# Optimization experiments

Hardware: AMD Instinct MI355X
Metric: run time of the kernel (lower is better)

The kernel has to match this reference:

```python
import jax, jax.numpy as jnp
import numpy as np

FRAME, LATENT, HIDDEN, GATE_H, EXPERTS = 267, 32, 256, 64, 6
BATCH = 4096
IN0 = LATENT + FRAME            # 299: decoder layer-0 input (z, c)
IN1 = LATENT + HIDDEN           # 288: decoder layer-1/2 input (z, h)
OUT = FRAME                     # num_future_predictions * frame_size


def _lin(key, fan_in, fan_out):
    b = np.sqrt(1.0 / fan_in)
    return jax.random.uniform(key, (fan_in, fan_out), jnp.float32, -b, b)


def setup_inputs() -> dict:
    key = jax.random.key(0)
    ks = jax.random.split(key, 16)
    d = {
        "x": jax.random.normal(ks[0], (BATCH, FRAME), jnp.float32),
        "c": jax.random.normal(ks[1], (BATCH, FRAME), jnp.float32),
        "eps": jax.random.normal(ks[2], (BATCH, LATENT), jnp.float32),
        # encoder
        "enc_w1": _lin(ks[3], 2 * FRAME, HIDDEN), "enc_b1": jnp.zeros((HIDDEN,), jnp.float32),
        "enc_w2": _lin(ks[4], FRAME + HIDDEN, HIDDEN), "enc_b2": jnp.zeros((HIDDEN,), jnp.float32),
        "enc_wmu": _lin(ks[5], FRAME + HIDDEN, LATENT), "enc_bmu": jnp.zeros((LATENT,), jnp.float32),
        "enc_wlv": _lin(ks[6], FRAME + HIDDEN, LATENT), "enc_blv": jnp.zeros((LATENT,), jnp.float32),
        # gate MLP
        "g_w0": _lin(ks[7], IN0, GATE_H), "g_b0": jnp.zeros((GATE_H,), jnp.float32),
        "g_w1": _lin(ks[8], GATE_H, GATE_H), "g_b1": jnp.zeros((GATE_H,), jnp.float32),
        "g_w2": _lin(ks[9], GATE_H, EXPERTS), "g_b2": jnp.zeros((EXPERTS,), jnp.float32),
        # expert-mixed decoder layers (kaiming-uniform-ish init, bias 0.01)
        "w0": jax.random.uniform(ks[10], (EXPERTS, IN0, HIDDEN), jnp.float32, -np.sqrt(6.0 / IN0), np.sqrt(6.0 / IN0)),
        "b0": jnp.full((EXPERTS, HIDDEN), 0.01, jnp.float32),
        "w1": jax.random.uniform(ks[11], (EXPERTS, IN1, HIDDEN), jnp.float32, -np.sqrt(6.0 / IN1), np.sqrt(6.0 / IN1)),
        "b1": jnp.full((EXPERTS, HIDDEN), 0.01, jnp.float32),
        "w2": jax.random.uniform(ks[12], (EXPERTS, IN1, OUT), jnp.float32, -np.sqrt(6.0 / IN1), np.sqrt(6.0 / IN1)),
        "b2": jnp.full((EXPERTS, OUT), 0.01, jnp.float32),
    }
    return d


def reference(x, c, eps,
              enc_w1, enc_b1, enc_w2, enc_b2, enc_wmu, enc_bmu, enc_wlv, enc_blv,
              g_w0, g_b0, g_w1, g_b1, g_w2, g_b2,
              w0, b0, w1, b1, w2, b2):
    elu = jax.nn.elu
    # --- encoder ---
    h1 = elu(jnp.concatenate([x, c], axis=1) @ enc_w1 + enc_b1)
    h2 = elu(jnp.concatenate([x, h1], axis=1) @ enc_w2 + enc_b2)
    s = jnp.concatenate([x, h2], axis=1)
    mu = s @ enc_wmu + enc_bmu
    logvar = s @ enc_wlv + enc_blv
    z = mu + eps * jnp.exp(0.5 * logvar)
    # --- gate ---
    zc = jnp.concatenate([z, c], axis=1)
    g = elu(zc @ g_w0 + g_b0)
    g = elu(g @ g_w1 + g_b1)
    coeff = jax.nn.softmax(g @ g_w2 + g_b2, axis=1)  # [N, E]
    # --- soft-MoE decoder: blended-weight per-sample GEMMs ---
    layer = c
    for w, b, act in ((w0, b0, elu), (w1, b1, elu), (w2, b2, None)):
        inp = jnp.concatenate([z, layer], axis=1)  # [N, Din]
        # out[n,o] = sum_e coeff[n,e] * (inp[n,:] @ w[e,:,o]) + coeff[n,:] @ b[:,o]
        out = jnp.einsum('ne,ni,eio->no', coeff, inp, w) + coeff @ b
        layer = act(out) if act is not None else out
    return layer, mu, logvar
```

## Files before the change

### kernel.cpp

```cpp
#include <hip/hip_runtime.h>
#include <hip/hip_bf16.h>
#include <math.h>

#define N_BATCH 4096
#define FRAME   267
#define LATENT  32
#define HIDDEN  256
#define GATE_H  64
#define EXPERTS 6

typedef __hip_bfloat16 bf16;
typedef __bf16  bf16x8 __attribute__((ext_vector_type(8)));
typedef float   f32x4  __attribute__((ext_vector_type(4)));

__device__ __forceinline__ float eluf(float v) { return (v > 0.f) ? v : (expf(v) - 1.f); }

#define MFMA(a, b, p) __builtin_amdgcn_mfma_f32_16x16x32_bf16((a), (b), (p), 0, 0, 0)

struct WEnt { const float* src; bf16* dst; int K, M, Mtot, mOff, Ksteps, Mtiles, cum; };
struct WTab { WEnt e[10]; int total; };

__global__ __launch_bounds__(256) void prep_kernel(
    const float* __restrict__ bmu, const float* __restrict__ blv,
    float* __restrict__ biasCat, WTab tab)
{
    const int tid = threadIdx.x, bid = blockIdx.x;
    if (bid == 0 && tid < 64)
        biasCat[tid] = (tid < 32) ? bmu[tid] : blv[tid - 32];

    __shared__ float tbuf[32][33];
    int i = 0;
    while (i < 9 && bid >= tab.e[i + 1].cum) ++i;
    const WEnt en = tab.e[i];
    const int t = bid - en.cum;
    const int perE = en.Ksteps * en.Mtiles;
    const int e = t / perE;
    const int rr = t - e * perE;
    const int mt = rr / en.Ksteps;
    const int ks = rr - mt * en.Ksteps;
    const int tx = tid & 31, ty = tid >> 5;
    const float* src = en.src + (size_t)e * en.K * en.M;
    #pragma unroll
    for (int i0 = 0; i0 < 32; i0 += 8) {
        const int k = ks * 32 + i0 + ty, m = mt * 32 + tx;
        tbuf[i0 + ty][tx] = (k < en.K && m < en.M) ? src[(size_t)k * en.M + m] : 0.f;
    }
    __syncthreads();
    bf16* dst = en.dst + ((size_t)(e * en.Ksteps + ks) * en.Mtot + en.mOff + mt * 32) * 32;
    #pragma unroll
    for (int i0 = 0; i0 < 32; i0 += 8)
        dst[(size_t)(i0 + ty) * 32 + tx] = __float2bfloat16(tbuf[tx][i0 + ty]);
}

__global__ __launch_bounds__(1024, 4) void fused_kernel(
    const float* __restrict__ x, const float* __restrict__ c,
    const float* __restrict__ eps,
    const bf16* __restrict__ We1, const float* __restrict__ eb1,
    const bf16* __restrict__ We2, const float* __restrict__ eb2,
    const bf16* __restrict__ Wml, const float* __restrict__ biasCat,
    const bf16* __restrict__ Wg0, const float* __restrict__ gb0,
    const bf16* __restrict__ Wg1, const float* __restrict__ gb1,
    const bf16* __restrict__ Wg2, const float* __restrict__ gb2,
    const bf16* __restrict__ W0, const float* __restrict__ b0,
    const bf16* __restrict__ W1, const float* __restrict__ b1,
    const bf16* __restrict__ W2, const float* __restrict__ b2,
    float* __restrict__ out_layer, float* __restrict__ out_mu,
    float* __restrict__ out_lv)
{
    __shared__ bf16  bufA[16 * 552];
    __shared__ bf16  bufB[16 * 552];
    __shared__ float sML[16 * 64];
    __shared__ bf16  sG1[16 * 72];
    __shared__ bf16  sG2[16 * 72];
    __shared__ float sLg[16 * 16];
    __shared__ float sCo[EXPERTS * 16];

    const int tid  = threadIdx.x;
    const int w    = tid >> 6, lane = tid & 63, ml = lane & 15, quad = lane >> 4;
    const int row0 = blockIdx.x * 16;

    {
        const float* xr = x + (size_t)(row0 + w) * FRAME;
        const float* cr = c + (size_t)(row0 + w) * FRAME;
        #pragma unroll
        for (int j = 0; j < 9; ++j) {
            const int col = lane + j * 64;
            if (col < 544) {
                float v = 0.f;
                if (col < FRAME)          v = xr[col];
                else if (col < 2 * FRAME) v = cr[col - FRAME];
                bufA[w * 552 + col] = __float2bfloat16(v);
            }
        }
    }
    __syncthreads();

    {
        const int col = 16 * w + ml;
        f32x4 pa = (f32x4){0,0,0,0}, pb = (f32x4){0,0,0,0};
        const bf16* wp = We1 + (size_t)col * 32 + quad * 8;
        #pragma unroll
        for (int ks = 0; ks < 16; ks += 2) {
            const bf16x8 a0 = *(const bf16x8*)(bufA + ml * 552 + ks * 32 + quad * 8);
            const bf16x8 a1 = *(const bf16x8*)(bufA + ml * 552 + (ks + 1) * 32 + quad * 8);
            pa = MFMA(a0, *(const bf16x8*)(wp + (size_t)ks * 256 * 32), pa);
            pb = MFMA(a1, *(const bf16x8*)(wp + (size_t)(ks + 1) * 256 * 32), pb);
        }
        {
            const bf16x8 a16 = *(const bf16x8*)(bufA + ml * 552 + 16 * 32 + quad * 8);
            pa = MFMA(a16, *(const bf16x8*)(wp + (size_t)16 * 256 * 32), pa);
        }
        const float bv = eb1[col];
        #pragma unroll
        for (int rg = 0; rg < 4; ++rg)
            bufB[(quad * 4 + rg) * 552 + 267 + col] =
                __float2bfloat16(eluf(pa[rg] + pb[rg] + bv));
        #pragma unroll
        for (int j = 0; j < 5; ++j) {
            const int cc = lane + j * 64;
            if (cc < 267) bufB[w * 552 + cc] = bufA[w * 552 + cc];
        }
        if (lane < 21) bufB[w * 552 + 523 + lane] = __float2bfloat16(0.f);
    }
    __syncthreads();

    {
        const int col = 16 * w + ml;
        f32x4 pa = (f32x4){0,0,0,0}, pb = (f32x4){0,0,0,0};
        const bf16* wp = We2 + (size_t)col * 32 + quad * 8;
        #pragma unroll
        for (int ks = 0; ks < 16; ks += 2) {
            const bf16x8 a0 = *(const bf16x8*)(bufB + ml * 552 + ks * 32 + quad * 8);
            const bf16x8 a1 = *(const bf16x8*)(bufB + ml * 552 + (ks + 1) * 32 + quad * 8);
            pa = MFMA(a0, *(const bf16x8*)(wp + (size_t)ks * 256 * 32), pa);
            pb = MFMA(a1, *(const bf16x8*)(wp + (size_t)(ks + 1) * 256 * 32), pb);
        }
        {
            const bf16x8 a16 = *(const bf16x8*)(bufB + ml * 552 + 16 * 32 + quad * 8);
            pa = MFMA(a16, *(const bf16x8*)(wp + (size_t)16 * 256 * 32), pa);
        }
        __syncthreads();
        const float bv = eb2[col];
        #pragma unroll
        for (int rg = 0; rg < 4; ++rg)
            bufB[(quad * 4 + rg) * 552 + 267 + col] =
                __float2bfloat16(eluf(pa[rg] + pb[rg] + bv));
    }
    __syncthreads();

    if (w < 4) {
        const int col = 16 * w + ml;
        f32x4 pa = (f32x4){0,0,0,0}, pb = (f32x4){0,0,0,0};
        const bf16* wp = Wml + (size_t)col * 32 + quad * 8;
        #pragma unroll
        for (int ks = 0; ks < 16; ks += 2) {
            const bf16x8 a0 = *(const bf16x8*)(bufB + ml * 552 + ks * 32 + quad * 8);
            const bf16x8 a1 = *(const bf16x8*)(bufB + ml * 552 + (ks + 1) * 32 + quad * 8);
            pa = MFMA(a0, *(const bf16x8*)(wp + (size_t)ks * 64 * 32), pa);
            pb = MFMA(a1, *(const bf16x8*)(wp + (size_t)(ks + 1) * 64 * 32), pb);
        }
        {
            const bf16x8 a16 = *(const bf16x8*)(bufB + ml * 552 + 16 * 32 + quad * 8);
            pa = MFMA(a16, *(const bf16x8*)(wp + (size_t)16 * 64 * 32), pa);
        }
        const float bv = biasCat[col];
        #pragma unroll
        for (int rg = 0; rg < 4; ++rg)
            sML[(quad * 4 + rg) * 64 + col] = pa[rg] + pb[rg] + bv;
    }
    __syncthreads();

    if (tid < 512) {
        const int r = tid >> 5, l = tid & 31;
        const float m  = sML[r * 64 + l];
        const float lv = sML[r * 64 + 32 + l];
        const int gi = (row0 + r) * LATENT + l;
        out_mu[gi] = m; out_lv[gi] = lv;
        const bf16 zb = __float2bfloat16(m + eps[gi] * expf(0.5f * lv));
        bufA[r * 552 + l] = zb;
        bufB[r * 552 + l] = zb;
        #pragma unroll
        for (int j = 0; j < 9; ++j) {
            const int col = 32 + l + j * 32;
            bf16 v = __float2bfloat16(0.f);
            if (col < 299) v = bufA[r * 552 + 267 + (col - 32)];
            bufB[r * 552 + col] = v;
        }
    }
    __syncthreads();

    {
        const int col = 16 * w + ml;
        bf16x8 av[10];
        #pragma unroll
        for (int ks = 0; ks < 10; ++ks)
            av[ks] = *(const bf16x8*)(bufB + ml * 552 + ks * 32 + quad * 8);

        if (w == 0) {
            #pragma unroll
            for (int t = 0; t < 4; ++t) {
                const int gc = 16 * t + ml;
                f32x4 p = (f32x4){0,0,0,0};
                const bf16* wp = Wg0 + (size_t)gc * 32 + quad * 8;
                #pragma unroll
                for (int ks = 0; ks < 10; ++ks)
                    p = MFMA(av[ks], *(const bf16x8*)(wp + (size_t)ks * 64 * 32), p);
                const float bv = gb0[gc];
                #pragma unroll
                for (int rg = 0; rg < 4; ++rg)
                    sG1[(quad * 4 + rg) * 72 + gc] = __float2bfloat16(eluf(p[rg] + bv));
            }
            #pragma unroll
            for (int t = 0; t < 4; ++t) {
                const int gc = 16 * t + ml;
                f32x4 p = (f32x4){0,0,0,0};
                const bf16* wp = Wg1 + (size_t)gc * 32 + quad * 8;
                #pragma unroll
                for (int ks = 0; ks < 2; ++ks)
                    p = MFMA(*(const bf16x8*)(sG1 + ml * 72 + ks * 32 + quad * 8),
                             *(const bf16x8*)(wp + (size_t)ks * 64 * 32), p);
                const float bv = gb1[gc];
                #pragma unroll
                for (int rg = 0; rg < 4; ++rg)
                    sG2[(quad * 4 + rg) * 72 + gc] = __float2bfloat16(eluf(p[rg] + bv));
            }
            {
                f32x4 p = (f32x4){0,0,0,0};
                const bf16* wp = Wg2 + (size_t)ml * 32 + quad * 8;
                #pragma unroll
                for (int ks = 0; ks < 2; ++ks)
                    p = MFMA(*(const bf16x8*)(sG2 + ml * 72 + ks * 32 + quad * 8),
                             *(const bf16x8*)(wp + (size_t)ks * 32 * 32), p);
                const float bv = (ml < EXPERTS) ? gb2[ml] : 0.f;
                #pragma unroll
                for (int rg = 0; rg < 4; ++rg)
                    sLg[(quad * 4 + rg) * 16 + ml] = p[rg] + bv;
            }
            if (lane < 16) {
                float v[EXPERTS];
                float m = -1e30f;
                #pragma unroll
                for (int i = 0; i < EXPERTS; ++i) { v[i] = sLg[lane * 16 + i]; m = fmaxf(m, v[i]); }
                float s = 0.f;
                #pragma unroll
                for (int i = 0; i < EXPERTS; ++i) { v[i] = expf(v[i] - m); s += v[i]; }
                const float inv = 1.f / s;
                #pragma unroll
                for (int i = 0; i < EXPERTS; ++i) sCo[i * 16 + lane] = v[i] * inv;
            }
        }

        f32x4 pe0, pe1, pe2, pe3, pe4, pe5;
        auto moe_part = [&](int e, f32x4& pe) {
            const bf16* wp = W0 + ((size_t)e * 10 * 256 + col) * 32 + quad * 8;
            f32x4 pa = (f32x4){0,0,0,0}, pb = (f32x4){0,0,0,0};
            #pragma unroll
            for (int ks = 0; ks < 10; ks += 2) {
                pa = MFMA(av[ks],     *(const bf16x8*)(wp + (size_t)ks * 256 * 32), pa);
                pb = MFMA(av[ks + 1], *(const bf16x8*)(wp + (size_t)(ks + 1) * 256 * 32), pb);
            }
            pe = pa + pb;
        };
        moe_part(0, pe0); moe_part(1, pe1); moe_part(2, pe2);
        moe_part(3, pe3); moe_part(4, pe4); moe_part(5, pe5);
        __syncthreads();

        f32x4 acc = (f32x4){0,0,0,0};
        auto blend = [&](const f32x4& p, int e) {
            const float bv = b0[e * 256 + col];
            #pragma unroll
            for (int rg = 0; rg < 4; ++rg)
                acc[rg] += sCo[e * 16 + quad * 4 + rg] * (p[rg] + bv);
        };
        blend(pe0, 0); blend(pe1, 1); blend(pe2, 2);
        blend(pe3, 3); blend(pe4, 4); blend(pe5, 5);
        #pragma unroll
        for (int rg = 0; rg < 4; ++rg)
            bufA[(quad * 4 + rg) * 552 + 32 + col] = __float2bfloat16(eluf(acc[rg]));
    }
    __syncthreads();

    {
        const int col = 16 * w + ml;
        bf16x8 av[9];
        #pragma unroll
        for (int ks = 0; ks < 9; ++ks)
            av[ks] = *(const bf16x8*)(bufA + ml * 552 + ks * 32 + quad * 8);
        f32x4 acc = (f32x4){0,0,0,0};
        #pragma unroll
        for (int e = 0; e < EXPERTS; ++e) {
            const bf16* wp = W1 + ((size_t)e * 9 * 256 + col) * 32 + quad * 8;
            f32x4 pa = (f32x4){0,0,0,0}, pb = (f32x4){0,0,0,0};
            #pragma unroll
            for (int ks = 0; ks < 8; ks += 2) {
                pa = MFMA(av[ks],     *(const bf16x8*)(wp + (size_t)ks * 256 * 32), pa);
                pb = MFMA(av[ks + 1], *(const bf16x8*)(wp + (size_t)(ks + 1) * 256 * 32), pb);
            }
            pa = MFMA(av[8], *(const bf16x8*)(wp + (size_t)8 * 256 * 32), pa);
            const float bv = b1[e * 256 + col];
            #pragma unroll
            for (int rg = 0; rg < 4; ++rg)
                acc[rg] += sCo[e * 16 + quad * 4 + rg] * (pa[rg] + pb[rg] + bv);
        }
        #pragma unroll
        for (int rg = 0; rg < 4; ++rg)
            bufB[(quad * 4 + rg) * 552 + 32 + col] = __float2bfloat16(eluf(acc[rg]));
    }
    __syncthreads();

    {
        bf16x8 av[9];
        #pragma unroll
        for (int ks = 0; ks < 9; ++ks)
            av[ks] = *(const bf16x8*)(bufB + ml * 552 + ks * 32 + quad * 8);
        for (int t = w; t < 18; t += 16) {
            const int col = 16 * t + ml;
            f32x4 acc = (f32x4){0,0,0,0};
            #pragma unroll
            for (int e = 0; e < EXPERTS; ++e) {
                const bf16* wp = W2 + ((size_t)e * 9 * 320 + col) * 32 + quad * 8;
                f32x4 pa = (f32x4){0,0,0,0}, pb = (f32x4){0,0,0,0};
                #pragma unroll
                for (int ks = 0; ks < 8; ks += 2) {
                    pa = MFMA(av[ks],     *(const bf16x8*)(wp + (size_t)ks * 320 * 32), pa);
                    pb = MFMA(av[ks + 1], *(const bf16x8*)(wp + (size_t)(ks + 1) * 320 * 32), pb);
                }
                pa = MFMA(av[8], *(const bf16x8*)(wp + (size_t)8 * 320 * 32), pa);
                const float bv = (col < FRAME) ? b2[e * FRAME + col] : 0.f;
                #pragma unroll
                for (int rg = 0; rg < 4; ++rg)
                    acc[rg] += sCo[e * 16 + quad * 4 + rg] * (pa[rg] + pb[rg] + bv);
            }
            if (col < FRAME) {
                #pragma unroll
                for (int rg = 0; rg < 4; ++rg)
                    out_layer[(size_t)(row0 + quad * 4 + rg) * FRAME + col] = acc[rg];
            }
        }
    }
}

extern "C" void kernel_launch(void* const* d_in, const int* in_sizes, int n_in,
                              void* d_out, int out_size, void* d_ws, size_t ws_size,
                              hipStream_t stream) {
    const float* x       = (const float*)d_in[0];
    const float* c       = (const float*)d_in[1];
    const float* eps     = (const float*)d_in[2];
    const float* enc_w1  = (const float*)d_in[3];
    const float* enc_b1  = (const float*)d_in[4];
    const float* enc_w2  = (const float*)d_in[5];
    const float* enc_b2  = (const float*)d_in[6];
    const float* enc_wmu = (const float*)d_in[7];
    const float* enc_bmu = (const float*)d_in[8];
    const float* enc_wlv = (const float*)d_in[9];
    const float* enc_blv = (const float*)d_in[10];
    const float* g_w0    = (const float*)d_in[11];
    const float* g_b0    = (const float*)d_in[12];
    const float* g_w1    = (const float*)d_in[13];
    const float* g_b1    = (const float*)d_in[14];
    const float* g_w2    = (const float*)d_in[15];
    const float* g_b2    = (const float*)d_in[16];
    const float* w0      = (const float*)d_in[17];
    const float* b0      = (const float*)d_in[18];
    const float* w1      = (const float*)d_in[19];
    const float* b1      = (const float*)d_in[20];
    const float* w2      = (const float*)d_in[21];
    const float* b2      = (const float*)d_in[22];

    float* out_layer = (float*)d_out;
    float* out_mu    = out_layer + (size_t)N_BATCH * FRAME;
    float* out_lv    = out_mu    + (size_t)N_BATCH * LATENT;

    char* p = (char*)d_ws;
    float* biasCat = (float*)p;  p += 64 * 4;
    bf16* Wt_e1 = (bf16*)p;      p += (size_t)17 * 256 * 32 * 2;
    bf16* Wt_e2 = (bf16*)p;      p += (size_t)17 * 256 * 32 * 2;
    bf16* Wt_ml = (bf16*)p;      p += (size_t)17 * 64 * 32 * 2;
    bf16* Wt_g0 = (bf16*)p;      p += (size_t)10 * 64 * 32 * 2;
    bf16* Wt_g1 = (bf16*)p;      p += (size_t)2 * 64 * 32 * 2;
    bf16* Wt_g2 = (bf16*)p;      p += (size_t)2 * 32 * 32 * 2;
    bf16* Wt_w0 = (bf16*)p;      p += (size_t)EXPERTS * 10 * 256 * 32 * 2;
    bf16* Wt_w1 = (bf16*)p;      p += (size_t)EXPERTS * 9 * 256 * 32 * 2;
    bf16* Wt_w2 = (bf16*)p;      p += (size_t)EXPERTS * 9 * 320 * 32 * 2;

    WTab tab;
    int cum = 0, n = 0;
    auto add = [&](const float* src, bf16* dst, int K, int M, int Mtot, int mOff, int E) {
        int Ksteps;
        if (K == 534 || K == 523) Ksteps = 17;
        else if (K == 299) Ksteps = 10;
        else if (K == 288) Ksteps = 9;
        else Ksteps = 2;
        const int Mtiles = (M + 31) / 32;
        tab.e[n] = {src, dst, K, M, Mtot, mOff, Ksteps, Mtiles, cum};
        cum += E * Ksteps * Mtiles;
        ++n;
    };
    add(enc_w1,  Wt_e1, 534, 256, 256, 0, 1);
    add(enc_w2,  Wt_e2, 523, 256, 256, 0, 1);
    add(enc_wmu, Wt_ml, 523, 32, 64, 0, 1);
    add(enc_wlv, Wt_ml, 523, 32, 64, 32, 1);
    add(g_w0,    Wt_g0, 299, 64, 64, 0, 1);
    add(g_w1,    Wt_g1, 64, 64, 64, 0, 1);
    add(g_w2,    Wt_g2, 64, 6, 32, 0, 1);
    add(w0,      Wt_w0, 299, 256, 256, 0, EXPERTS);
    add(w1,      Wt_w1, 288, 256, 256, 0, EXPERTS);
    add(w2,      Wt_w2, 288, 267, 320, 0, EXPERTS);
    tab.total = cum;

    prep_kernel<<<dim3(cum), dim3(256), 0, stream>>>(enc_bmu, enc_blv, biasCat, tab);

    fused_kernel<<<dim3(N_BATCH / 16), dim3(1024), 0, stream>>>(
        x, c, eps,
        Wt_e1, enc_b1, Wt_e2, enc_b2, Wt_ml, biasCat,
        Wt_g0, g_b0, Wt_g1, g_b1, Wt_g2, g_b2,
        Wt_w0, b0, Wt_w1, b1, Wt_w2, b2,
        out_layer, out_mu, out_lv);
}
```

Baseline: 178.0 us.

## Software-pipeline weight loads via rotating register ring and rebalance small GEMM stages

Every MFMA loop now keeps an 8-deep rotating register ring of weight fragments, so global weight loads run ahead of the MFMAs that consume them, and A fragments are read from LDS on demand instead of being preloaded. The mu/logvar projection is split along K across all 16 waves with partial sums reduced in shared memory, replacing the version that used only 4 waves. The gate layer-0 GEMM is spread over 4 waves and overlapped with the first half of the layer-0 expert MFMAs, which are issued before the softmax coefficients are ready. The last-layer column-tile loop now stops at 17 tiles instead of 18, dropping a fully padded tile. The trade-off is more register pressure from the ring buffers and extra shared memory for the partial sums.

After: 166.9 us. -6.2%, faster.

```diff
diff --git a/kernel.cpp b/kernel.cpp
--- a/kernel.cpp
+++ b/kernel.cpp
@@ -69,7 +69,7 @@
 {
     __shared__ bf16  bufA[16 * 552];
     __shared__ bf16  bufB[16 * 552];
-    __shared__ float sML[16 * 64];
+    __shared__ float sMLp[4][16 * 64];
     __shared__ bf16  sG1[16 * 72];
     __shared__ bf16  sG2[16 * 72];
     __shared__ float sLg[16 * 16];
@@ -97,24 +97,21 @@
 
     {
         const int col = 16 * w + ml;
-        f32x4 pa = (f32x4){0,0,0,0}, pb = (f32x4){0,0,0,0};
-        const bf16* wp = We1 + (size_t)col * 32 + quad * 8;
-        #pragma unroll
-        for (int ks = 0; ks < 16; ks += 2) {
-            const bf16x8 a0 = *(const bf16x8*)(bufA + ml * 552 + ks * 32 + quad * 8);
-            const bf16x8 a1 = *(const bf16x8*)(bufA + ml * 552 + (ks + 1) * 32 + quad * 8);
-            pa = MFMA(a0, *(const bf16x8*)(wp + (size_t)ks * 256 * 32), pa);
-            pb = MFMA(a1, *(const bf16x8*)(wp + (size_t)(ks + 1) * 256 * 32), pb);
-        }
-        {
-            const bf16x8 a16 = *(const bf16x8*)(bufA + ml * 552 + 16 * 32 + quad * 8);
-            pa = MFMA(a16, *(const bf16x8*)(wp + (size_t)16 * 256 * 32), pa);
+        const bf16* wq = We1 + (size_t)col * 32 + quad * 8;
+        f32x4 acc = (f32x4){0,0,0,0};
+        bf16x8 bb[8];
+        #pragma unroll
+        for (int j = 0; j < 8; ++j) bb[j] = *(const bf16x8*)(wq + (size_t)j * 8192);
+        #pragma unroll
+        for (int u = 0; u < 17; ++u) {
+            const bf16x8 b = bb[u & 7];
+            if (u + 8 < 17) bb[u & 7] = *(const bf16x8*)(wq + (size_t)(u + 8) * 8192);
+            acc = MFMA(*(const bf16x8*)(bufA + ml * 552 + u * 32 + quad * 8), b, acc);
         }
         const float bv = eb1[col];
         #pragma unroll
         for (int rg = 0; rg < 4; ++rg)
-            bufB[(quad * 4 + rg) * 552 + 267 + col] =
-                __float2bfloat16(eluf(pa[rg] + pb[rg] + bv));
+            bufB[(quad * 4 + rg) * 552 + 267 + col] = __float2bfloat16(eluf(acc[rg] + bv));
         #pragma unroll
         for (int j = 0; j < 5; ++j) {
             const int cc = lane + j * 64;
@@ -126,54 +123,50 @@
 
     {
         const int col = 16 * w + ml;
-        f32x4 pa = (f32x4){0,0,0,0}, pb = (f32x4){0,0,0,0};
-        const bf16* wp = We2 + (size_t)col * 32 + quad * 8;
-        #pragma unroll
-        for (int ks = 0; ks < 16; ks += 2) {
-            const bf16x8 a0 = *(const bf16x8*)(bufB + ml * 552 + ks * 32 + quad * 8);
-            const bf16x8 a1 = *(const bf16x8*)(bufB + ml * 552 + (ks + 1) * 32 + quad * 8);
-            pa = MFMA(a0, *(const bf16x8*)(wp + (size_t)ks * 256 * 32), pa);
-            pb = MFMA(a1, *(const bf16x8*)(wp + (size_t)(ks + 1) * 256 * 32), pb);
-        }
-        {
-            const bf16x8 a16 = *(const bf16x8*)(bufB + ml * 552 + 16 * 32 + quad * 8);
-            pa = MFMA(a16, *(const bf16x8*)(wp + (size_t)16 * 256 * 32), pa);
+        const bf16* wq = We2 + (size_t)col * 32 + quad * 8;
+        f32x4 acc = (f32x4){0,0,0,0};
+        bf16x8 bb[8];
+        #pragma unroll
+        for (int j = 0; j < 8; ++j) bb[j] = *(const bf16x8*)(wq + (size_t)j * 8192);
+        #pragma unroll
+        for (int u = 0; u < 17; ++u) {
+            const bf16x8 b = bb[u & 7];
+            if (u + 8 < 17) bb[u & 7] = *(const bf16x8*)(wq + (size_t)(u + 8) * 8192);
+            acc = MFMA(*(const bf16x8*)(bufB + ml * 552 + u * 32 + quad * 8), b, acc);
         }
         __syncthreads();
         const float bv = eb2[col];
         #pragma unroll
         for (int rg = 0; rg < 4; ++rg)
-            bufB[(quad * 4 + rg) * 552 + 267 + col] =
-                __float2bfloat16(eluf(pa[rg] + pb[rg] + bv));
-    }
-    __syncthreads();
-
-    if (w < 4) {
-        const int col = 16 * w + ml;
-        f32x4 pa = (f32x4){0,0,0,0}, pb = (f32x4){0,0,0,0};
-        const bf16* wp = Wml + (size_t)col * 32 + quad * 8;
-        #pragma unroll
-        for (int ks = 0; ks < 16; ks += 2) {
-            const bf16x8 a0 = *(const bf16x8*)(bufB + ml * 552 + ks * 32 + quad * 8);
-            const bf16x8 a1 = *(const bf16x8*)(bufB + ml * 552 + (ks + 1) * 32 + quad * 8);
-            pa = MFMA(a0, *(const bf16x8*)(wp + (size_t)ks * 64 * 32), pa);
-            pb = MFMA(a1, *(const bf16x8*)(wp + (size_t)(ks + 1) * 64 * 32), pb);
-        }
-        {
-            const bf16x8 a16 = *(const bf16x8*)(bufB + ml * 552 + 16 * 32 + quad * 8);
-            pa = MFMA(a16, *(const bf16x8*)(wp + (size_t)16 * 64 * 32), pa);
-        }
-        const float bv = biasCat[col];
+            bufB[(quad * 4 + rg) * 552 + 267 + col] = __float2bfloat16(eluf(acc[rg] + bv));
+    }
+    __syncthreads();
+
+    {
+        const int t = w & 3, kg = w >> 2;
+        const int col = 16 * t + ml;
+        const int k0 = kg * 4, k1 = (kg == 3) ? 17 : kg * 4 + 4;
+        const bf16* wq = Wml + (size_t)col * 32 + quad * 8;
+        f32x4 p = (f32x4){0,0,0,0};
+        #pragma unroll
+        for (int u = 0; u < 5; ++u) {
+            const int ks = k0 + u;
+            if (ks < k1)
+                p = MFMA(*(const bf16x8*)(bufB + ml * 552 + ks * 32 + quad * 8),
+                         *(const bf16x8*)(wq + (size_t)ks * 2048), p);
+        }
         #pragma unroll
         for (int rg = 0; rg < 4; ++rg)
-            sML[(quad * 4 + rg) * 64 + col] = pa[rg] + pb[rg] + bv;
+            sMLp[kg][(quad * 4 + rg) * 64 + col] = p[rg];
     }
     __syncthreads();
 
     if (tid < 512) {
         const int r = tid >> 5, l = tid & 31;
-        const float m  = sML[r * 64 + l];
-        const float lv = sML[r * 64 + 32 + l];
+        const float m  = sMLp[0][r * 64 + l] + sMLp[1][r * 64 + l]
+                       + sMLp[2][r * 64 + l] + sMLp[3][r * 64 + l] + biasCat[l];
+        const float lv = sMLp[0][r * 64 + 32 + l] + sMLp[1][r * 64 + 32 + l]
+                       + sMLp[2][r * 64 + 32 + l] + sMLp[3][r * 64 + 32 + l] + biasCat[32 + l];
         const int gi = (row0 + r) * LATENT + l;
         out_mu[gi] = m; out_lv[gi] = lv;
         const bf16 zb = __float2bfloat16(m + eps[gi] * expf(0.5f * lv));
@@ -191,46 +184,59 @@
 
     {
         const int col = 16 * w + ml;
-        bf16x8 av[10];
-        #pragma unroll
-        for (int ks = 0; ks < 10; ++ks)
-            av[ks] = *(const bf16x8*)(bufB + ml * 552 + ks * 32 + quad * 8);
+        const bf16* wq = W0 + (size_t)col * 32 + quad * 8;
+        f32x4 pe[6] = {(f32x4){0,0,0,0}, (f32x4){0,0,0,0}, (f32x4){0,0,0,0},
+                       (f32x4){0,0,0,0}, (f32x4){0,0,0,0}, (f32x4){0,0,0,0}};
+
+        if (w < 4) {
+            const int gc = 16 * w + ml;
+            const bf16* gq = Wg0 + (size_t)gc * 32 + quad * 8;
+            f32x4 p = (f32x4){0,0,0,0};
+            #pragma unroll
+            for (int ks = 0; ks < 10; ++ks)
+                p = MFMA(*(const bf16x8*)(bufB + ml * 552 + ks * 32 + quad * 8),
+                         *(const bf16x8*)(gq + (size_t)ks * 2048), p);
+            const float bv = gb0[gc];
+            #pragma unroll
+            for (int rg = 0; rg < 4; ++rg)
+                sG1[(quad * 4 + rg) * 72 + gc] = __float2bfloat16(eluf(p[rg] + bv));
+        }
+        {
+            bf16x8 bb[8];
+            #pragma unroll
+            for (int j = 0; j < 8; ++j) bb[j] = *(const bf16x8*)(wq + (size_t)j * 8192);
+            #pragma unroll
+            for (int v = 0; v < 30; ++v) {
+                const bf16x8 b = bb[v & 7];
+                if (v + 8 < 30) bb[v & 7] = *(const bf16x8*)(wq + (size_t)(v + 8) * 8192);
+                pe[v / 10] = MFMA(*(const bf16x8*)(bufB + ml * 552 + (v % 10) * 32 + quad * 8),
+                                  b, pe[v / 10]);
+            }
+        }
+        __syncthreads();
 
         if (w == 0) {
             #pragma unroll
             for (int t = 0; t < 4; ++t) {
                 const int gc = 16 * t + ml;
+                const bf16* gq = Wg1 + (size_t)gc * 32 + quad * 8;
                 f32x4 p = (f32x4){0,0,0,0};
-                const bf16* wp = Wg0 + (size_t)gc * 32 + quad * 8;
-                #pragma unroll
-                for (int ks = 0; ks < 10; ++ks)
-                    p = MFMA(av[ks], *(const bf16x8*)(wp + (size_t)ks * 64 * 32), p);
-                const float bv = gb0[gc];
-                #pragma unroll
-                for (int rg = 0; rg < 4; ++rg)
-                    sG1[(quad * 4 + rg) * 72 + gc] = __float2bfloat16(eluf(p[rg] + bv));
-            }
-            #pragma unroll
-            for (int t = 0; t < 4; ++t) {
-                const int gc = 16 * t + ml;
-                f32x4 p = (f32x4){0,0,0,0};
-                const bf16* wp = Wg1 + (size_t)gc * 32 + quad * 8;
                 #pragma unroll
                 for (int ks = 0; ks < 2; ++ks)
                     p = MFMA(*(const bf16x8*)(sG1 + ml * 72 + ks * 32 + quad * 8),
-                             *(const bf16x8*)(wp + (size_t)ks * 64 * 32), p);
+                             *(const bf16x8*)(gq + (size_t)ks * 2048), p);
                 const float bv = gb1[gc];
                 #pragma unroll
                 for (int rg = 0; rg < 4; ++rg)
                     sG2[(quad * 4 + rg) * 72 + gc] = __float2bfloat16(eluf(p[rg] + bv));
             }
             {
+                const bf16* gq = Wg2 + (size_t)ml * 32 + quad * 8;
                 f32x4 p = (f32x4){0,0,0,0};
-                const bf16* wp = Wg2 + (size_t)ml * 32 + quad * 8;
                 #pragma unroll
                 for (int ks = 0; ks < 2; ++ks)
                     p = MFMA(*(const bf16x8*)(sG2 + ml * 72 + ks * 32 + quad * 8),
-                             *(const bf16x8*)(wp + (size_t)ks * 32 * 32), p);
+                             *(const bf16x8*)(gq + (size_t)ks * 1024), p);
                 const float bv = (ml < EXPERTS) ? gb2[ml] : 0.f;
                 #pragma unroll
                 for (int rg = 0; rg < 4; ++rg)
@@ -249,31 +255,29 @@
                 for (int i = 0; i < EXPERTS; ++i) sCo[i * 16 + lane] = v[i] * inv;
             }
         }
-
-        f32x4 pe0, pe1, pe2, pe3, pe4, pe5;
-        auto moe_part = [&](int e, f32x4& pe) {
-            const bf16* wp = W0 + ((size_t)e * 10 * 256 + col) * 32 + quad * 8;
-            f32x4 pa = (f32x4){0,0,0,0}, pb = (f32x4){0,0,0,0};
-            #pragma unroll
-            for (int ks = 0; ks < 10; ks += 2) {
-                pa = MFMA(av[ks],     *(const bf16x8*)(wp + (size_t)ks * 256 * 32), pa);
-                pb = MFMA(av[ks + 1], *(const bf16x8*)(wp + (size_t)(ks + 1) * 256 * 32), pb);
-            }
-            pe = pa + pb;
-        };
-        moe_part(0, pe0); moe_part(1, pe1); moe_part(2, pe2);
-        moe_part(3, pe3); moe_part(4, pe4); moe_part(5, pe5);
+        {
+            bf16x8 bb[8];
+            #pragma unroll
+            for (int j = 0; j < 8; ++j) bb[j] = *(const bf16x8*)(wq + (size_t)(30 + j) * 8192);
+            #pragma unroll
+            for (int v = 0; v < 30; ++v) {
+                const bf16x8 b = bb[v & 7];
+                if (v + 8 < 30) bb[v & 7] = *(const bf16x8*)(wq + (size_t)(30 + v + 8) * 8192);
+                const int u = 30 + v;
+                pe[u / 10] = MFMA(*(const bf16x8*)(bufB + ml * 552 + (u % 10) * 32 + quad * 8),
+                                  b, pe[u / 10]);
+            }
+        }
         __syncthreads();
 
         f32x4 acc = (f32x4){0,0,0,0};
-        auto blend = [&](const f32x4& p, int e) {
+        #pragma unroll
+        for (int e = 0; e < EXPERTS; ++e) {
             const float bv = b0[e * 256 + col];
             #pragma unroll
             for (int rg = 0; rg < 4; ++rg)
-                acc[rg] += sCo[e * 16 + quad * 4 + rg] * (p[rg] + bv);
-        };
-        blend(pe0, 0); blend(pe1, 1); blend(pe2, 2);
-        blend(pe3, 3); blend(pe4, 4); blend(pe5, 5);
+                acc[rg] += sCo[e * 16 + quad * 4 + rg] * (pe[e][rg] + bv);
+        }
         #pragma unroll
         for (int rg = 0; rg < 4; ++rg)
             bufA[(quad * 4 + rg) * 552 + 32 + col] = __float2bfloat16(eluf(acc[rg]));
@@ -282,25 +286,26 @@
 
     {
         const int col = 16 * w + ml;
-        bf16x8 av[9];
-        #pragma unroll
-        for (int ks = 0; ks < 9; ++ks)
-            av[ks] = *(const bf16x8*)(bufA + ml * 552 + ks * 32 + quad * 8);
+        const bf16* wq = W1 + (size_t)col * 32 + quad * 8;
+        f32x4 pe[6] = {(f32x4){0,0,0,0}, (f32x4){0,0,0,0}, (f32x4){0,0,0,0},
+                       (f32x4){0,0,0,0}, (f32x4){0,0,0,0}, (f32x4){0,0,0,0}};
+        bf16x8 bb[8];
+        #pragma unroll
+        for (int j = 0; j < 8; ++j) bb[j] = *(const bf16x8*)(wq + (size_t)j * 8192);
+        #pragma unroll
+        for (int u = 0; u < 54; ++u) {
+            const bf16x8 b = bb[u & 7];
+            if (u + 8 < 54) bb[u & 7] = *(const bf16x8*)(wq + (size_t)(u + 8) * 8192);
+            pe[u / 9] = MFMA(*(const bf16x8*)(bufA + ml * 552 + (u % 9) * 32 + quad * 8),
+                             b, pe[u / 9]);
+        }
         f32x4 acc = (f32x4){0,0,0,0};
         #pragma unroll
         for (int e = 0; e < EXPERTS; ++e) {
-            const bf16* wp = W1 + ((size_t)e * 9 * 256 + col) * 32 + quad * 8;
-            f32x4 pa = (f32x4){0,0,0,0}, pb = (f32x4){0,0,0,0};
-            #pragma unroll
-            for (int ks = 0; ks < 8; ks += 2) {
-                pa = MFMA(av[ks],     *(const bf16x8*)(wp + (size_t)ks * 256 * 32), pa);
-                pb = MFMA(av[ks + 1], *(const bf16x8*)(wp + (size_t)(ks + 1) * 256 * 32), pb);
-            }
-            pa = MFMA(av[8], *(const bf16x8*)(wp + (size_t)8 * 256 * 32), pa);
             const float bv = b1[e * 256 + col];
             #pragma unroll
             for (int rg = 0; rg < 4; ++rg)
-                acc[rg] += sCo[e * 16 + quad * 4 + rg] * (pa[rg] + pb[rg] + bv);
+                acc[rg] += sCo[e * 16 + quad * 4 + rg] * (pe[e][rg] + bv);
         }
         #pragma unroll
         for (int rg = 0; rg < 4; ++rg)
@@ -309,27 +314,28 @@
     __syncthreads();
 
     {
-        bf16x8 av[9];
-        #pragma unroll
-        for (int ks = 0; ks < 9; ++ks)
-            av[ks] = *(const bf16x8*)(bufB + ml * 552 + ks * 32 + quad * 8);
-        for (int t = w; t < 18; t += 16) {
+        for (int t = w; t < 17; t += 16) {
             const int col = 16 * t + ml;
+            const bf16* wq = W2 + (size_t)col * 32 + quad * 8;
+            f32x4 pe[6] = {(f32x4){0,0,0,0}, (f32x4){0,0,0,0}, (f32x4){0,0,0,0},
+                           (f32x4){0,0,0,0}, (f32x4){0,0,0,0}, (f32x4){0,0,0,0}};
+            bf16x8 bb[8];
+            #pragma unroll
+            for (int j = 0; j < 8; ++j) bb[j] = *(const bf16x8*)(wq + (size_t)j * 10240);
+            #pragma unroll
+            for (int u = 0; u < 54; ++u) {
+                const bf16x8 b = bb[u & 7];
+                if (u + 8 < 54) bb[u & 7] = *(const bf16x8*)(wq + (size_t)(u + 8) * 10240);
+                pe[u / 9] = MFMA(*(const bf16x8*)(bufB + ml * 552 + (u % 9) * 32 + quad * 8),
+                                 b, pe[u / 9]);
+            }
             f32x4 acc = (f32x4){0,0,0,0};
             #pragma unroll
             for (int e = 0; e < EXPERTS; ++e) {
-                const bf16* wp = W2 + ((size_t)e * 9 * 320 + col) * 32 + quad * 8;
-                f32x4 pa = (f32x4){0,0,0,0}, pb = (f32x4){0,0,0,0};
-                #pragma unroll
-                for (int ks = 0; ks < 8; ks += 2) {
-                    pa = MFMA(av[ks],     *(const bf16x8*)(wp + (size_t)ks * 320 * 32), pa);
-                    pb = MFMA(av[ks + 1], *(const bf16x8*)(wp + (size_t)(ks + 1) * 320 * 32), pb);
-                }
-                pa = MFMA(av[8], *(const bf16x8*)(wp + (size_t)8 * 320 * 32), pa);
                 const float bv = (col < FRAME) ? b2[e * FRAME + col] : 0.f;
                 #pragma unroll
                 for (int rg = 0; rg < 4; ++rg)
-                    acc[rg] += sCo[e * 16 + quad * 4 + rg] * (pa[rg] + pb[rg] + bv);
+                    acc[rg] += sCo[e * 16 + quad * 4 + rg] * (pe[e][rg] + bv);
             }
             if (col < FRAME) {
                 #pragma unroll
```
